# Kernel tuning notes

Hardware: AMD Instinct MI355X
Metric: run time of the kernel (lower is better)

The kernel has to match this reference:

```python
import jax, jax.numpy as jnp
import numpy as np

B, SEQ, DIM = 1, 720, 2048
N_HEADS, HEAD_DIM = 16, 128
CACHE_SIZE = 11520
SINK_TOKENS = 720
CURRENT_START = 11520
FRAME_SEQLEN = 720
EPS = 1e-6


def _rmsnorm(x, w, eps=EPS):
    # WanRMSNorm: x * rsqrt(mean(x^2) + eps) * weight
    return x * jax.lax.rsqrt(jnp.mean(x * x, axis=-1, keepdims=True) + eps) * w


def _rope(x, cos, sin):
    # x: [b, s, n, d]; pairs are consecutive (reshape(..., d//2, 2)) as in causal_rope_apply
    b, s, n, d = x.shape
    xp = x.reshape(b, s, n, d // 2, 2)
    xr, xi = xp[..., 0], xp[..., 1]
    c = cos[None, :, None, :]
    sn = sin[None, :, None, :]
    out = jnp.stack([xr * c - xi * sn, xr * sn + xi * c], axis=-1)
    return out.reshape(b, s, n, d)


def _make_freqs():
    # precompute_freqs_i_t_only: head_dim//2 = 64 complex freqs; first 22 temporal
    # (rope_t_params with dim = 128 - 4*(128//6) = 44 -> 22 freqs), h/w parts use
    # table row 0 -> angle 0 (identity).
    f, h, w = 1, 20, 36
    t0 = CURRENT_START // FRAME_SEQLEN  # 16
    c = HEAD_DIM // 2
    dim_t = 44
    inv = 1.0 / (10000.0 ** (np.arange(0, dim_t, 2, dtype=np.float64) / dim_t))  # [22]
    ang_t = np.outer(np.arange(f, dtype=np.float64) + t0, inv)  # [f, 22]
    ang = np.zeros((f, h, w, c), dtype=np.float64)
    ang[..., : inv.shape[0]] = ang_t[:, None, None, :]
    ang = ang.reshape(f * h * w, c)
    return np.cos(ang).astype(np.float32), np.sin(ang).astype(np.float32)


def setup_inputs() -> dict:
    key = jax.random.key(0)
    ks = jax.random.split(key, 8)
    w_scale = 0.02
    cos, sin = _make_freqs()
    return {
        "x": jax.random.normal(ks[0], (B, SEQ, DIM), jnp.float32),
        "q_w": jax.random.normal(ks[1], (DIM, DIM), jnp.float32) * w_scale,
        "q_b": jnp.zeros((DIM,), jnp.float32),
        "k_w": jax.random.normal(ks[2], (DIM, DIM), jnp.float32) * w_scale,
        "k_b": jnp.zeros((DIM,), jnp.float32),
        "v_w": jax.random.normal(ks[3], (DIM, DIM), jnp.float32) * w_scale,
        "v_b": jnp.zeros((DIM,), jnp.float32),
        "o_w": jax.random.normal(ks[4], (DIM, DIM), jnp.float32) * w_scale,
        "o_b": jnp.zeros((DIM,), jnp.float32),
        "norm_q_w": jnp.ones((DIM,), jnp.float32),
        "norm_k_w": jnp.ones((DIM,), jnp.float32),
        "cache_k": jax.random.normal(ks[5], (B, CACHE_SIZE, N_HEADS, HEAD_DIM), jnp.float32),
        "cache_v": jax.random.normal(ks[6], (B, CACHE_SIZE, N_HEADS, HEAD_DIM), jnp.float32),
        "freqs_cos": jnp.asarray(cos),
        "freqs_sin": jnp.asarray(sin),
        "current_start": CURRENT_START,
        "frame_seqlen": FRAME_SEQLEN,
        "sink_tokens": SINK_TOKENS,
    }


def reference(x, q_w, q_b, k_w, k_b, v_w, v_b, o_w, o_b, norm_q_w, norm_k_w,
              cache_k, cache_v, freqs_cos, freqs_sin,
              current_start, frame_seqlen, sink_tokens):
    b, s, _ = x.shape
    n, d = cache_k.shape[2], cache_k.shape[3]
    # qkv projections with qk RMSNorm
    q = _rmsnorm(x @ q_w.T + q_b, norm_q_w).reshape(b, s, n, d)
    k = _rmsnorm(x @ k_w.T + k_b, norm_k_w).reshape(b, s, n, d)
    v = (x @ v_w.T + v_b).reshape(b, s, n, d)
    # RoPE on new q/k (causal_rope_apply with precomputed freqs_i)
    rq = _rope(q, freqs_cos, freqs_sin)
    rk = _rope(k, freqs_cos, freqs_sin)
    # rolling KV-cache write (contiguous case: local_end > local_start)
    cache_size = cache_k.shape[1]
    rolling = cache_size - sink_tokens
    local_start = (current_start - sink_tokens) % rolling + sink_tokens
    k_all = jax.lax.dynamic_update_slice(cache_k, rk, (0, local_start, 0, 0))
    v_all = jax.lax.dynamic_update_slice(cache_v, v, (0, local_start, 0, 0))
    # full-cache attention branch (cache_size == sink + max_attention, current_end >= cache_size)
    scale = d ** -0.5
    scores = jnp.einsum('bqnd,bknd->bnqk', rq, k_all) * scale  # [b, n, s, cache]
    probs = jax.nn.softmax(scores, axis=-1)
    out = jnp.einsum('bnqk,bknd->bqnd', probs, v_all).reshape(b, s, n * d)
    return out @ o_w.T + o_b
```

## Files before the change

### kernel.cpp

```cpp
#include <hip/hip_runtime.h>

#define SEQ 720
#define DIM 2048
#define NH 16
#define HD 128
#define CACHE 11520
#define KSP 8
#define LOG2E 1.4426950408889634f
#define SM_SCALE 0.08838834764831845f
#define CSCL (SM_SCALE * LOG2E)

typedef unsigned short u16;
typedef unsigned int u32;
typedef __bf16 bf8_t __attribute__((ext_vector_type(8)));
typedef float f4 __attribute__((ext_vector_type(4)));

__device__ __forceinline__ float bf2f(u16 v) {
    union { u32 u; float f; } t; t.u = ((u32)v) << 16; return t.f;
}
__device__ __forceinline__ u16 f2bf(float f) {
    union { float f; u32 u; } t; t.f = f;
    u32 u = t.u;
    return (u16)((u + 0x7fffu + ((u >> 16) & 1u)) >> 16);
}
__device__ __forceinline__ u16 f2bf_fast(float f) {
    __bf16 h = (__bf16)f;
    return __builtin_bit_cast(u16, h);
}
__device__ __forceinline__ bf8_t ld_bf8(const u16* p) {
    const u16* pa = (const u16*)__builtin_assume_aligned(p, 16);
    bf8_t r;
    __builtin_memcpy(&r, pa, 16);
    return r;
}
__device__ __forceinline__ void st8(u16* p, const u16* v) {
    __builtin_memcpy((u16*)__builtin_assume_aligned(p, 16), v, 16);
}
__device__ __forceinline__ void ld8_cvt(const void* base, size_t off, int f32, u16* dst) {
    if (f32) {
        const float* p = (const float*)base + off;
        float v[8];
        __builtin_memcpy(v, (const float*)__builtin_assume_aligned(p, 16), 32);
        #pragma unroll
        for (int i = 0; i < 8; i++) dst[i] = f2bf(v[i]);
    } else {
        const u16* p = (const u16*)base + off;
        __builtin_memcpy(dst, (const u16*)__builtin_assume_aligned(p, 16), 16);
    }
}
__device__ __forceinline__ float ld1(const void* base, size_t off, int f32) {
    return f32 ? ((const float*)base)[off] : bf2f(((const u16*)base)[off]);
}
__device__ __forceinline__ int ls_from(const int* cs_p, const int* sink_p) {
    const int cs = cs_p[0], sink = sink_p[0];
    const int rolling = CACHE - sink;
    int ls = (cs - sink) % rolling + sink;
    if (ls > CACHE - SEQ) ls = CACHE - SEQ;
    return ls;
}

__device__ __forceinline__ void cp16_lds(u16* lds, const u16* g) {
    __builtin_amdgcn_global_load_lds(
        (const __attribute__((address_space(1))) void*)g,
        (__attribute__((address_space(3))) void*)lds,
        16, 0, 0);
}

__global__ __launch_bounds__(256) void detect_kernel(const void* probe, int* flag) {
    __shared__ int cnt[256];
    const int tid = threadIdx.x;
    const u16* p = (const u16*)probe;
    int bad = 0;
    for (int i = tid; i < 4096; i += 256) {
        int e = (p[i] >> 7) & 0xFF;
        bad += (e < 0x60 || e > 0x90) ? 1 : 0;
    }
    cnt[tid] = bad;
    __syncthreads();
    if (tid == 0) {
        int s = 0;
        for (int i = 0; i < 256; i++) s += cnt[i];
        flag[0] = (s > 256) ? 1 : 0;
    }
}

__device__ __forceinline__ void gemm2_body(const void* __restrict__ A, int aF32,
                                           const void* __restrict__ W,
                                           const void* __restrict__ bias, int wF32,
                                           void* __restrict__ C, int cF32, int M)
{
    __shared__ __align__(16) u16 As[64 * 64];
    __shared__ __align__(16) u16 Bs[128 * 64];
    const int tid = threadIdx.x;
    const int wv = tid >> 6, lane = tid & 63, quad = lane >> 4, l16 = lane & 15;
    const int n0 = blockIdx.x * 128, m0 = blockIdx.y * 64;
    const int wr = (wv & 1) * 32, wc = (wv >> 1) * 64;

    f4 acc[2][4];
    #pragma unroll
    for (int i = 0; i < 2; i++)
        #pragma unroll
        for (int j = 0; j < 4; j++)
            acc[i][j] = f4{0.f, 0.f, 0.f, 0.f};

    const int srow = tid >> 3, scb = tid & 7;

    for (int kb = 0; kb < DIM / 64; kb++) {
        const int k0 = kb * 64;
        u16 avt[2][8], bvt[4][8];
        #pragma unroll
        for (int i = 0; i < 2; i++) {
            const int row = srow + 32 * i;
            int gm = m0 + row; if (gm >= M) gm = M - 1;
            ld8_cvt(A, (size_t)gm * DIM + k0 + scb * 8, aF32, avt[i]);
        }
        #pragma unroll
        for (int i = 0; i < 4; i++) {
            const int row = srow + 32 * i;
            ld8_cvt(W, (size_t)(n0 + row) * DIM + k0 + scb * 8, wF32, bvt[i]);
        }
        __syncthreads();
        #pragma unroll
        for (int i = 0; i < 2; i++) {
            const int row = srow + 32 * i;
            st8(&As[row * 64 + ((scb ^ (row & 7)) * 8)], avt[i]);
        }
        #pragma unroll
        for (int i = 0; i < 4; i++) {
            const int row = srow + 32 * i;
            st8(&Bs[row * 64 + ((scb ^ (row & 7)) * 8)], bvt[i]);
        }
        __syncthreads();
        #pragma unroll
        for (int s = 0; s < 2; s++) {
            bf8_t af[2], bfr[4];
            #pragma unroll
            for (int i = 0; i < 2; i++) {
                const int m = wr + i * 16 + l16;
                af[i]  = ld_bf8(&As[m * 64 + (((s * 4 + quad) ^ (m & 7)) * 8)]);
            }
            #pragma unroll
            for (int i = 0; i < 4; i++) {
                const int n = wc + i * 16 + l16;
                bfr[i] = ld_bf8(&Bs[n * 64 + (((s * 4 + quad) ^ (n & 7)) * 8)]);
            }
            #pragma unroll
            for (int mi = 0; mi < 2; mi++)
                #pragma unroll
                for (int nj = 0; nj < 4; nj++)
                    acc[mi][nj] = __builtin_amdgcn_mfma_f32_16x16x32_bf16(af[mi], bfr[nj], acc[mi][nj], 0, 0, 0);
        }
    }

    #pragma unroll
    for (int mi = 0; mi < 2; mi++) {
        const int rowb = m0 + wr + mi * 16 + quad * 4;
        #pragma unroll
        for (int r = 0; r < 4; r++) {
            if (rowb + r < M) {
                #pragma unroll
                for (int nj = 0; nj < 4; nj++) {
                    const int col = n0 + wc + nj * 16 + l16;
                    float v = acc[mi][nj][r] + ld1(bias, col, wF32);
                    if (cF32) ((float*)C)[(size_t)(rowb + r) * DIM + col] = v;
                    else      ((u16*)C)[(size_t)(rowb + r) * DIM + col] = f2bf(v);
                }
            }
        }
    }
}

__global__ __launch_bounds__(256) void gemm2_qkv_kernel(
    const void* __restrict__ X,
    const void* __restrict__ w0, const void* __restrict__ w1, const void* __restrict__ w2,
    const void* __restrict__ b0, const void* __restrict__ b1, const void* __restrict__ b2,
    u16* __restrict__ o0, u16* __restrict__ o1, u16* __restrict__ o2,
    const int* __restrict__ dflag, int M)
{
    const int z = blockIdx.z;
    const void* W = (z == 0) ? w0 : (z == 1) ? w1 : w2;
    const void* B = (z == 0) ? b0 : (z == 1) ? b1 : b2;
    u16* O = (z == 0) ? o0 : (z == 1) ? o1 : o2;
    const int f32 = dflag[0];
    gemm2_body(X, f32, W, B, f32, O, 0, M);
}

__global__ __launch_bounds__(256) void gemm2_o_kernel(
    const u16* __restrict__ X, const void* __restrict__ W,
    const void* __restrict__ B, void* __restrict__ O,
    const int* __restrict__ dflag, int M)
{
    const int f32 = dflag[0];
    gemm2_body(X, 0, W, B, f32, O, f32, M);
}

__global__ __launch_bounds__(256) void normrope_kernel(
    u16* __restrict__ qbuf, u16* __restrict__ kbuf,
    const void* __restrict__ nqw, const void* __restrict__ nkw,
    const void* __restrict__ fcos, const void* __restrict__ fsin,
    const int* __restrict__ dflag)
{
    const int f32 = dflag[0];
    const int row = blockIdx.x, z = blockIdx.y;
    const int tid = threadIdx.x, lane = tid & 63, wvi = tid >> 6;
    u16* buf = ((z == 0) ? qbuf : kbuf) + (size_t)row * DIM + tid * 8;
    u16 in[8];
    __builtin_memcpy(in, (const u16*)__builtin_assume_aligned(buf, 16), 16);
    float x[8];
    #pragma unroll
    for (int i = 0; i < 8; i++) x[i] = bf2f(in[i]);
    float ss = 0.f;
    #pragma unroll
    for (int i = 0; i < 8; i++) ss += x[i] * x[i];
    ss += __shfl_xor(ss, 32); ss += __shfl_xor(ss, 16); ss += __shfl_xor(ss, 8);
    ss += __shfl_xor(ss, 4);  ss += __shfl_xor(ss, 2);  ss += __shfl_xor(ss, 1);
    __shared__ float red[4];
    if (lane == 0) red[wvi] = ss;
    __syncthreads();
    const float rinv = rsqrtf((red[0] + red[1] + red[2] + red[3]) * (1.0f / DIM) + 1e-6f);
    const void* wn = (z == 0) ? nqw : nkw;
    float y[8];
    #pragma unroll
    for (int i = 0; i < 8; i++) y[i] = x[i] * rinv * ld1(wn, tid * 8 + i, f32);
    const int dd = (tid * 8) & (HD - 1);
    const int cb = row * 64 + (dd >> 1);
    u16 outv[8];
    #pragma unroll
    for (int p = 0; p < 4; p++) {
        float cv = ld1(fcos, cb + p, f32), sv = ld1(fsin, cb + p, f32);
        float xr = y[2 * p], xi = y[2 * p + 1];
        outv[2 * p]     = f2bf(xr * cv - xi * sv);
        outv[2 * p + 1] = f2bf(xr * sv + xi * cv);
    }
    __builtin_memcpy((u16*)__builtin_assume_aligned(buf, 16), outv, 16);
}

__global__ __launch_bounds__(256) void cvtk_kernel(
    const void* __restrict__ cache_k, const u16* __restrict__ kr,
    u16* __restrict__ Kb, const int* __restrict__ cs_p,
    const int* __restrict__ sink_p, const int* __restrict__ dflag)
{
    const int f32 = dflag[0];
    const int kt = blockIdx.x, h = blockIdx.y, tid = threadIdx.x;
    const int ls = ls_from(cs_p, sink_p);
    #pragma unroll
    for (int i = 0; i < 8; i++) {
        const int idx = i * 2048 + tid * 8;
        const int key = kt * 128 + (idx >> 7);
        const int d0 = idx & 127;
        u16 tmp[8];
        if (key >= ls && key < ls + SEQ)
            ld8_cvt(kr, (size_t)(key - ls) * DIM + h * HD + d0, 0, tmp);
        else
            ld8_cvt(cache_k, (size_t)key * DIM + h * HD + d0, f32, tmp);
        st8(&Kb[((size_t)h * CACHE + key) * HD + d0], tmp);
    }
}

__device__ __forceinline__ int swz(int ky, int cb) {
    return (cb ^ (ky >> 3) ^ ((ky & 7) << 1)) & 15;
}

__global__ __launch_bounds__(256) void cvtv_kernel(
    const void* __restrict__ cache_v, const u16* __restrict__ vr,
    u16* __restrict__ Vt, const int* __restrict__ cs_p,
    const int* __restrict__ sink_p, const int* __restrict__ dflag)
{
    __shared__ __align__(16) u16 Vtile[128 * 128];
    const int f32 = dflag[0];
    const int kt = blockIdx.x, h = blockIdx.y, tid = threadIdx.x;
    const int ls = ls_from(cs_p, sink_p);
    #pragma unroll
    for (int i = 0; i < 8; i++) {
        const int idx = i * 2048 + tid * 8;
        const int ky = idx >> 7;
        const int d0 = idx & 127;
        const int key = kt * 128 + ky;
        u16 tmp[8];
        if (key >= ls && key < ls + SEQ)
            ld8_cvt(vr, (size_t)(key - ls) * DIM + h * HD + d0, 0, tmp);
        else
            ld8_cvt(cache_v, (size_t)key * DIM + h * HD + d0, f32, tmp);
        st8(&Vtile[ky * 128 + swz(ky, d0 >> 3) * 8], tmp);
    }
    __syncthreads();
    #pragma unroll
    for (int i = 0; i < 8; i++) {
        const int oidx = i * 2048 + tid * 8;
        const int d = oidx >> 7;
        const int k8 = oidx & 127;
        u16 o[8];
        #pragma unroll
        for (int j = 0; j < 8; j++) {
            const int ky = k8 + j;
            o[j] = Vtile[ky * 128 + swz(ky, d >> 3) * 8 + (d & 7)];
        }
        st8(&Vt[((size_t)h * HD + d) * CACHE + kt * 128 + k8], o);
    }
}

__global__ __launch_bounds__(256, 3) void attn2_kernel(
    const u16* __restrict__ qr, const u16* __restrict__ Kb, const u16* __restrict__ Vt,
    float* __restrict__ pO, float* __restrict__ pLp)
{
    __shared__ __align__(16) u16 Klds[2][32 * 128];
    __shared__ __align__(16) u16 Vlds[3][128 * 32];
    __shared__ __align__(16) u16 Ps[4][32 * 40];
    const int tid = threadIdx.x;
    const int wvi = tid >> 6, lane = tid & 63, quad = lane >> 4, l16 = lane & 15;
    const int kc = blockIdx.x, qb = blockIdx.y, h = blockIdx.z;
    const int q0 = qb * 128 + wvi * 32;
    const int kch = CACHE / KSP;
    const int ktiles = kch / 32;

    bf8_t aQ[2][4];
    #pragma unroll
    for (int mi = 0; mi < 2; mi++) {
        int qrow = q0 + mi * 16 + l16; if (qrow >= SEQ) qrow = SEQ - 1;
        const u16* qp = qr + (size_t)qrow * DIM + h * HD + quad * 8;
        #pragma unroll
        for (int dc = 0; dc < 4; dc++) aQ[mi][dc] = ld_bf8(qp + dc * 32);
    }

    f4 O[2][8];
    float lsum[2][4];
    #pragma unroll
    for (int mi = 0; mi < 2; mi++) {
        #pragma unroll
        for (int dc = 0; dc < 8; dc++) O[mi][dc] = f4{0.f, 0.f, 0.f, 0.f};
        #pragma unroll
        for (int r = 0; r < 4; r++) lsum[mi][r] = 0.f;
    }

    const u16* kbase = Kb + ((size_t)h * CACHE + (size_t)kc * kch) * HD;
    const u16* vbase = Vt + (size_t)h * HD * CACHE + (size_t)kc * kch;

    const int s0 = tid, s1 = tid + 256;
    const int koff0 = (s0 >> 4) * HD + (((s0 & 15) ^ ((s0 >> 4) & 15)) * 8);
    const int koff1 = (s1 >> 4) * HD + (((s1 & 15) ^ ((s1 >> 4) & 15)) * 8);
    const size_t voff0 = (size_t)(s0 >> 2) * CACHE
                       + (((s0 & 3) ^ ((s0 >> 2) & 3) ^ ((s0 >> 4) & 3)) * 8);
    const size_t voff1 = (size_t)(s1 >> 2) * CACHE
                       + (((s1 & 3) ^ ((s1 >> 2) & 3) ^ ((s1 >> 4) & 3)) * 8);

    auto stageK = [&](int t, int b) {
        const u16* kp = kbase + (size_t)t * 32 * HD;
        cp16_lds(&Klds[b][wvi * 512], kp + koff0);
        cp16_lds(&Klds[b][2048 + wvi * 512], kp + koff1);
    };
    auto stageV = [&](int t, int b) {
        const u16* vp = vbase + t * 32;
        cp16_lds(&Vlds[b][wvi * 512], vp + voff0);
        cp16_lds(&Vlds[b][2048 + wvi * 512], vp + voff1);
    };
    auto qkt = [&](int b, f4 sc[2][2]) {
        bf8_t kf[8];
        #pragma unroll
        for (int dc = 0; dc < 4; dc++) {
            const int g8 = ((quad + 4 * dc) ^ l16) * 8;
            kf[dc]     = ld_bf8(&Klds[b][l16 * HD + g8]);
            kf[4 + dc] = ld_bf8(&Klds[b][(16 + l16) * HD + g8]);
        }
        #pragma unroll
        for (int mi = 0; mi < 2; mi++) { sc[mi][0] = f4{0.f,0.f,0.f,0.f}; sc[mi][1] = f4{0.f,0.f,0.f,0.f}; }
        #pragma unroll
        for (int dc = 0; dc < 4; dc++) {
            #pragma unroll
            for (int mi = 0; mi < 2; mi++) {
                sc[mi][0] = __builtin_amdgcn_mfma_f32_16x16x32_bf16(aQ[mi][dc], kf[dc],     sc[mi][0], 0, 0, 0);
                sc[mi][1] = __builtin_amdgcn_mfma_f32_16x16x32_bf16(aQ[mi][dc], kf[4 + dc], sc[mi][1], 0, 0, 0);
            }
        }
    };
    auto smax = [&](const f4 sc[2][2]) {
        #pragma unroll
        for (int mi = 0; mi < 2; mi++) {
            #pragma unroll
            for (int r = 0; r < 4; r++) {
                float p0 = exp2f(sc[mi][0][r] * CSCL);
                float p1 = exp2f(sc[mi][1][r] * CSCL);
                lsum[mi][r] += p0 + p1;
                const int prow = mi * 16 + quad * 4 + r;
                Ps[wvi][prow * 40 + l16]      = f2bf_fast(p0);
                Ps[wvi][prow * 40 + 16 + l16] = f2bf_fast(p1);
            }
        }
    };
    const int vq8 = (quad ^ (l16 & 3) ^ (l16 >> 2)) * 8;
    auto pv = [&](bf8_t ap0, bf8_t ap1, int vb) {
        bf8_t vf[8];
        #pragma unroll
        for (int dc = 0; dc < 8; dc++)
            vf[dc] = ld_bf8(&Vlds[vb][(dc * 16 + l16) * 32 + vq8]);
        #pragma unroll
        for (int dc = 0; dc < 8; dc++) {
            O[0][dc] = __builtin_amdgcn_mfma_f32_16x16x32_bf16(ap0, vf[dc], O[0][dc], 0, 0, 0);
            O[1][dc] = __builtin_amdgcn_mfma_f32_16x16x32_bf16(ap1, vf[dc], O[1][dc], 0, 0, 0);
        }
    };

    stageK(0, 0);
    stageV(0, 0);
    __syncthreads();

    {
        stageK(1, 1);
        stageV(1, 1);
        f4 sc[2][2];
        qkt(0, sc);
        smax(sc);
        __syncthreads();
    }

    int vr = 0, vs = 2;
    for (int t = 1; t < ktiles; t++) {
        const int kb = t & 1;
        if (t + 1 < ktiles) {
            stageK(t + 1, kb ^ 1);
            stageV(t + 1, vs);
        }
        f4 sc[2][2];
        qkt(kb, sc);
        bf8_t ap0 = ld_bf8(&Ps[wvi][l16 * 40 + quad * 8]);
        bf8_t ap1 = ld_bf8(&Ps[wvi][(16 + l16) * 40 + quad * 8]);
        smax(sc);
        pv(ap0, ap1, vr);
        __syncthreads();
        vr = (vr == 2) ? 0 : vr + 1;
        vs = (vs == 2) ? 0 : vs + 1;
    }

    {
        bf8_t ap0 = ld_bf8(&Ps[wvi][l16 * 40 + quad * 8]);
        bf8_t ap1 = ld_bf8(&Ps[wvi][(16 + l16) * 40 + quad * 8]);
        pv(ap0, ap1, vr);
    }

    #pragma unroll
    for (int mi = 0; mi < 2; mi++)
        #pragma unroll
        for (int r = 0; r < 4; r++) {
            float s = lsum[mi][r];
            s += __shfl_xor(s, 1); s += __shfl_xor(s, 2);
            s += __shfl_xor(s, 4); s += __shfl_xor(s, 8);
            lsum[mi][r] = s;
        }
    #pragma unroll
    for (int mi = 0; mi < 2; mi++) {
        #pragma unroll
        for (int r = 0; r < 4; r++) {
            const int q = q0 + mi * 16 + quad * 4 + r;
            if (q < SEQ) {
                const size_t rb = (size_t)(h * SEQ + q);
                const size_t pb = (rb * KSP + kc) * HD;
                #pragma unroll
                for (int dc = 0; dc < 8; dc++)
                    pO[pb + dc * 16 + l16] = O[mi][dc][r];
                if (l16 == 0) pLp[rb * KSP + kc] = lsum[mi][r];
            }
        }
    }
}

__global__ __launch_bounds__(128) void combine2_kernel(
    const float* __restrict__ pO, const float* __restrict__ pLp,
    u16* __restrict__ attn)
{
    const int q = blockIdx.x, h = blockIdx.y, d = threadIdx.x;
    const size_t rb = (size_t)(h * SEQ + q);
    float num = 0.f, den = 0.f;
    #pragma unroll
    for (int s = 0; s < KSP; s++) {
        num += pO[(rb * KSP + s) * HD + d];
        den += pLp[rb * KSP + s];
    }
    attn[(size_t)q * DIM + h * HD + d] = f2bf(num / den);
}

extern "C" void kernel_launch(void* const* d_in, const int* in_sizes, int n_in,
                              void* d_out, int out_size, void* d_ws, size_t ws_size,
                              hipStream_t stream)
{
    const void* x    = d_in[0];
    const void* q_w  = d_in[1];
    const void* q_b  = d_in[2];
    const void* k_w  = d_in[3];
    const void* k_b  = d_in[4];
    const void* v_w  = d_in[5];
    const void* v_b  = d_in[6];
    const void* o_w  = d_in[7];
    const void* o_b  = d_in[8];
    const void* nqw  = d_in[9];
    const void* nkw  = d_in[10];
    const void* cK   = d_in[11];
    const void* cV   = d_in[12];
    const void* fcos = d_in[13];
    const void* fsin = d_in[14];
    const int* cs_p   = (const int*)d_in[15];
    const int* sink_p = (const int*)d_in[17];

    char* ws = (char*)d_ws;
    const size_t SZB  = (size_t)SEQ * DIM * 2;
    const size_t KBsz = (size_t)NH * CACHE * HD * 2;
    const size_t PO1  = (size_t)NH * SEQ * HD * 4;

    int*  dflag = (int*)ws;
    u16*  q_l   = (u16*)(ws + 256);
    u16*  k_l   = (u16*)(ws + 256 + SZB);
    u16*  v_l   = (u16*)(ws + 256 + 2 * SZB);
    u16*  attn  = (u16*)(ws + 256 + 3 * SZB);
    char* pbase = ws + 256 + 4 * SZB;
    u16*   Kb = (u16*)pbase;
    u16*   Vt = (u16*)(pbase + KBsz);
    float* pO = (float*)(pbase + 2 * KBsz);
    float* pLp = (float*)v_l;

    dim3 blk(256);
    detect_kernel<<<1, blk, 0, stream>>>(q_w, dflag);

    gemm2_qkv_kernel<<<dim3(16, 12, 3), blk, 0, stream>>>(
        x, q_w, k_w, v_w, q_b, k_b, v_b, q_l, k_l, v_l, dflag, SEQ);
    normrope_kernel<<<dim3(SEQ, 2), blk, 0, stream>>>(
        q_l, k_l, nqw, nkw, fcos, fsin, dflag);

    cvtk_kernel<<<dim3(CACHE / 128, NH), blk, 0, stream>>>(cK, k_l, Kb, cs_p, sink_p, dflag);
    cvtv_kernel<<<dim3(CACHE / 128, NH), blk, 0, stream>>>(cV, v_l, Vt, cs_p, sink_p, dflag);
    attn2_kernel<<<dim3(KSP, 6, NH), blk, 0, stream>>>(q_l, Kb, Vt, pO, pLp);
    combine2_kernel<<<dim3(SEQ, NH), dim3(128), 0, stream>>>(pO, pLp, attn);

    gemm2_o_kernel<<<dim3(16, 12, 1), blk, 0, stream>>>(
        attn, o_w, o_b, d_out, dflag, SEQ);
}
```

Measured before the change: 608.0 us.

## Pre-convert GEMM operands to bf16 and double-buffer LDS via async copies

Adds a conversion kernel that turns the f32 weights and activations into bf16 workspace buffers before the projection GEMMs. The GEMM body then loads tiles straight into double-buffered LDS with direct global-to-LDS copies, so the next tile is fetched while the current one is multiplied, and it uses a faster bf16 rounding. This is meant to cut conversion work inside the GEMM loop and hide global load latency. The cost is extra launches and a full pass over the weights each call, plus reuse of the pO scratch region for the converted weights.

New measurement: 493.9 us. 1.23x faster.

```diff
diff --git a/kernel.cpp b/kernel.cpp
--- a/kernel.cpp
+++ b/kernel.cpp
@@ -84,13 +84,30 @@
     }
 }
 
-__device__ __forceinline__ void gemm2_body(const void* __restrict__ A, int aF32,
-                                           const void* __restrict__ W,
-                                           const void* __restrict__ bias, int wF32,
+__global__ __launch_bounds__(256) void cvt3_kernel(
+    const void* __restrict__ s0, const void* __restrict__ s1, const void* __restrict__ s2,
+    u16* __restrict__ d0, u16* __restrict__ d1, u16* __restrict__ d2,
+    int n, const int* __restrict__ dflag)
+{
+    const int f32 = dflag[0];
+    const int z = blockIdx.y;
+    const void* s = (z == 0) ? s0 : (z == 1) ? s1 : s2;
+    u16* d = (z == 0) ? d0 : (z == 1) ? d1 : d2;
+    const int idx = (blockIdx.x * 256 + threadIdx.x) * 8;
+    if (idx < n) {
+        u16 t[8];
+        ld8_cvt(s, idx, f32, t);
+        st8(d + idx, t);
+    }
+}
+
+__device__ __forceinline__ void gemm2_body(const u16* __restrict__ A,
+                                           const u16* __restrict__ W,
+                                           const void* __restrict__ bias, int bF32,
                                            void* __restrict__ C, int cF32, int M)
 {
-    __shared__ __align__(16) u16 As[64 * 64];
-    __shared__ __align__(16) u16 Bs[128 * 64];
+    __shared__ __align__(16) u16 As[2][64 * 64];
+    __shared__ __align__(16) u16 Bs[2][128 * 64];
     const int tid = threadIdx.x;
     const int wv = tid >> 6, lane = tid & 63, quad = lane >> 4, l16 = lane & 15;
     const int n0 = blockIdx.x * 128, m0 = blockIdx.y * 64;
@@ -103,46 +120,50 @@
         for (int j = 0; j < 4; j++)
             acc[i][j] = f4{0.f, 0.f, 0.f, 0.f};
 
-    const int srow = tid >> 3, scb = tid & 7;
+    size_t aoff[2];
+    #pragma unroll
+    for (int i = 0; i < 2; i++) {
+        const int s = wv * 128 + i * 64 + lane;
+        const int row = s >> 3, g = s & 7;
+        int gm = m0 + row; if (gm >= M) gm = M - 1;
+        aoff[i] = (size_t)gm * DIM + ((g ^ (row & 7)) * 8);
+    }
+    size_t boff[4];
+    #pragma unroll
+    for (int i = 0; i < 4; i++) {
+        const int s = wv * 256 + i * 64 + lane;
+        const int row = s >> 3, g = s & 7;
+        boff[i] = (size_t)(n0 + row) * DIM + ((g ^ (row & 7)) * 8);
+    }
+
+    auto stage = [&](int kb, int b) {
+        const int k0 = kb * 64;
+        #pragma unroll
+        for (int i = 0; i < 2; i++)
+            cp16_lds(&As[b][wv * 1024 + i * 512], A + aoff[i] + k0);
+        #pragma unroll
+        for (int i = 0; i < 4; i++)
+            cp16_lds(&Bs[b][wv * 2048 + i * 512], W + boff[i] + k0);
+    };
+
+    stage(0, 0);
+    __syncthreads();
 
     for (int kb = 0; kb < DIM / 64; kb++) {
-        const int k0 = kb * 64;
-        u16 avt[2][8], bvt[4][8];
-        #pragma unroll
-        for (int i = 0; i < 2; i++) {
-            const int row = srow + 32 * i;
-            int gm = m0 + row; if (gm >= M) gm = M - 1;
-            ld8_cvt(A, (size_t)gm * DIM + k0 + scb * 8, aF32, avt[i]);
-        }
-        #pragma unroll
-        for (int i = 0; i < 4; i++) {
-            const int row = srow + 32 * i;
-            ld8_cvt(W, (size_t)(n0 + row) * DIM + k0 + scb * 8, wF32, bvt[i]);
-        }
-        __syncthreads();
-        #pragma unroll
-        for (int i = 0; i < 2; i++) {
-            const int row = srow + 32 * i;
-            st8(&As[row * 64 + ((scb ^ (row & 7)) * 8)], avt[i]);
-        }
-        #pragma unroll
-        for (int i = 0; i < 4; i++) {
-            const int row = srow + 32 * i;
-            st8(&Bs[row * 64 + ((scb ^ (row & 7)) * 8)], bvt[i]);
-        }
-        __syncthreads();
+        const int b = kb & 1;
+        if (kb + 1 < DIM / 64) stage(kb + 1, b ^ 1);
         #pragma unroll
         for (int s = 0; s < 2; s++) {
             bf8_t af[2], bfr[4];
             #pragma unroll
             for (int i = 0; i < 2; i++) {
                 const int m = wr + i * 16 + l16;
-                af[i]  = ld_bf8(&As[m * 64 + (((s * 4 + quad) ^ (m & 7)) * 8)]);
+                af[i]  = ld_bf8(&As[b][m * 64 + (((s * 4 + quad) ^ (m & 7)) * 8)]);
             }
             #pragma unroll
             for (int i = 0; i < 4; i++) {
                 const int n = wc + i * 16 + l16;
-                bfr[i] = ld_bf8(&Bs[n * 64 + (((s * 4 + quad) ^ (n & 7)) * 8)]);
+                bfr[i] = ld_bf8(&Bs[b][n * 64 + (((s * 4 + quad) ^ (n & 7)) * 8)]);
             }
             #pragma unroll
             for (int mi = 0; mi < 2; mi++)
@@ -150,6 +171,7 @@
                 for (int nj = 0; nj < 4; nj++)
                     acc[mi][nj] = __builtin_amdgcn_mfma_f32_16x16x32_bf16(af[mi], bfr[nj], acc[mi][nj], 0, 0, 0);
         }
+        __syncthreads();
     }
 
     #pragma unroll
@@ -161,9 +183,9 @@
                 #pragma unroll
                 for (int nj = 0; nj < 4; nj++) {
                     const int col = n0 + wc + nj * 16 + l16;
-                    float v = acc[mi][nj][r] + ld1(bias, col, wF32);
+                    float v = acc[mi][nj][r] + ld1(bias, col, bF32);
                     if (cF32) ((float*)C)[(size_t)(rowb + r) * DIM + col] = v;
-                    else      ((u16*)C)[(size_t)(rowb + r) * DIM + col] = f2bf(v);
+                    else      ((u16*)C)[(size_t)(rowb + r) * DIM + col] = f2bf_fast(v);
                 }
             }
         }
@@ -171,27 +193,26 @@
 }
 
 __global__ __launch_bounds__(256) void gemm2_qkv_kernel(
-    const void* __restrict__ X,
-    const void* __restrict__ w0, const void* __restrict__ w1, const void* __restrict__ w2,
+    const u16* __restrict__ X,
+    const u16* __restrict__ w0, const u16* __restrict__ w1, const u16* __restrict__ w2,
     const void* __restrict__ b0, const void* __restrict__ b1, const void* __restrict__ b2,
     u16* __restrict__ o0, u16* __restrict__ o1, u16* __restrict__ o2,
     const int* __restrict__ dflag, int M)
 {
     const int z = blockIdx.z;
-    const void* W = (z == 0) ? w0 : (z == 1) ? w1 : w2;
+    const u16* W = (z == 0) ? w0 : (z == 1) ? w1 : w2;
     const void* B = (z == 0) ? b0 : (z == 1) ? b1 : b2;
     u16* O = (z == 0) ? o0 : (z == 1) ? o1 : o2;
-    const int f32 = dflag[0];
-    gemm2_body(X, f32, W, B, f32, O, 0, M);
+    gemm2_body(X, W, B, dflag[0], O, 0, M);
 }
 
 __global__ __launch_bounds__(256) void gemm2_o_kernel(
-    const u16* __restrict__ X, const void* __restrict__ W,
+    const u16* __restrict__ X, const u16* __restrict__ W,
     const void* __restrict__ B, void* __restrict__ O,
     const int* __restrict__ dflag, int M)
 {
     const int f32 = dflag[0];
-    gemm2_body(X, 0, W, B, f32, O, f32, M);
+    gemm2_body(X, W, B, f32, O, f32, M);
 }
 
 __global__ __launch_bounds__(256) void normrope_kernel(
@@ -502,7 +523,6 @@
     char* ws = (char*)d_ws;
     const size_t SZB  = (size_t)SEQ * DIM * 2;
     const size_t KBsz = (size_t)NH * CACHE * HD * 2;
-    const size_t PO1  = (size_t)NH * SEQ * HD * 4;
 
     int*  dflag = (int*)ws;
     u16*  q_l   = (u16*)(ws + 256);
@@ -515,11 +535,21 @@
     float* pO = (float*)(pbase + 2 * KBsz);
     float* pLp = (float*)v_l;
 
+    u16* Wq = (u16*)pO;
+    u16* Wk = Wq + (size_t)DIM * DIM;
+    u16* Wv = Wk + (size_t)DIM * DIM;
+    u16* x_bf = Wv + (size_t)DIM * DIM;
+    u16* Wo = (u16*)pO;
+
     dim3 blk(256);
     detect_kernel<<<1, blk, 0, stream>>>(q_w, dflag);
 
+    cvt3_kernel<<<dim3(DIM * DIM / 2048, 3), blk, 0, stream>>>(
+        q_w, k_w, v_w, Wq, Wk, Wv, DIM * DIM, dflag);
+    cvt3_kernel<<<dim3(SEQ * DIM / 2048, 1), blk, 0, stream>>>(
+        x, x, x, x_bf, x_bf, x_bf, SEQ * DIM, dflag);
     gemm2_qkv_kernel<<<dim3(16, 12, 3), blk, 0, stream>>>(
-        x, q_w, k_w, v_w, q_b, k_b, v_b, q_l, k_l, v_l, dflag, SEQ);
+        x_bf, Wq, Wk, Wv, q_b, k_b, v_b, q_l, k_l, v_l, dflag, SEQ);
     normrope_kernel<<<dim3(SEQ, 2), blk, 0, stream>>>(
         q_l, k_l, nqw, nkw, fcos, fsin, dflag);
 
@@ -528,6 +558,8 @@
     attn2_kernel<<<dim3(KSP, 6, NH), blk, 0, stream>>>(q_l, Kb, Vt, pO, pLp);
     combine2_kernel<<<dim3(SEQ, NH), dim3(128), 0, stream>>>(pO, pLp, attn);
 
+    cvt3_kernel<<<dim3(DIM * DIM / 2048, 1), blk, 0, stream>>>(
+        o_w, o_w, o_w, Wo, Wo, Wo, DIM * DIM, dflag);
     gemm2_o_kernel<<<dim3(16, 12, 1), blk, 0, stream>>>(
-        attn, o_w, o_b, d_out, dflag, SEQ);
-}
+        attn, Wo, o_b, d_out, dflag, SEQ);
+}
```
